# Optimization experiments

Measured on AMD Instinct MI355X. Metric: run time of the kernel, lower is better.

Reference implementation:

```python
import jax, jax.numpy as jnp
import numpy as np

MARGIN = 5.0
B, D, N_CLASSES = 384, 256, 64


def _pairwise_euclidean(emb):
    # sentence-transformers BatchHardTripletLossDistanceFunction.eucledian_distance
    dot = emb @ emb.T                          # [B,B]
    sq = jnp.diag(dot)                         # [B]
    d2 = sq[None, :] - 2.0 * dot + sq[:, None]
    d2 = jnp.maximum(d2, 0.0)
    zero = (d2 == 0.0).astype(emb.dtype)
    # add eps where zero to keep sqrt grad finite, then zero those entries
    return (1.0 - zero) * jnp.sqrt(d2 + zero * 1e-16)


def _triplet_mask(labels):
    # valid (i,j,k): distinct indices, label[i]==label[j], label[i]!=label[k]
    n = labels.shape[0]
    neq = ~jnp.eye(n, dtype=bool)
    distinct = neq[:, :, None] & neq[:, None, :] & neq[None, :, :]
    leq = labels[:, None] == labels[None, :]
    valid = leq[:, :, None] & (~leq[:, None, :])
    return valid & distinct


def setup_inputs() -> dict:
    key = jax.random.key(0)
    k1, k2 = jax.random.split(key)
    emb = jax.random.normal(k1, (B, D), dtype=jnp.float32)
    labels = jax.random.randint(k2, (B,), 0, N_CLASSES, dtype=jnp.int64)
    return {"emb": emb, "labels": labels}


def reference(emb, labels):
    pdist = _pairwise_euclidean(emb)                      # [B,B]
    # anchor-positive dist minus anchor-negative dist + margin -> [B,B,B]
    tl = pdist[:, :, None] - pdist[:, None, :] + MARGIN
    mask = _triplet_mask(labels).astype(tl.dtype)
    tl = jnp.maximum(mask * tl, 0.0)
    num_pos = jnp.sum(tl > 1e-16).astype(tl.dtype)
    return jnp.sum(tl) / (num_pos + 1e-16)
```

## Files before the change

### kernel.cpp

```cpp
#include <hip/hip_runtime.h>
#include <math.h>

#define MARGIN 5.0f
#define NB 384
#define ND 256
#define NBLK 192
#define APB 2
#define DC 32
#define NCH (ND / DC)
#define RP 33
#define MAGIC_A 0x51B7A5E1u
#define MAGIC_B 0xC3D2E1F0u

__global__ __launch_bounds__(384) void fused_kernel(const float* __restrict__ emb,
                                                    const int* __restrict__ labels,
                                                    unsigned long long* __restrict__ slotA,
                                                    unsigned long long* __restrict__ slotB,
                                                    float* __restrict__ out) {
    __shared__ float s_tile[NB][RP];
    __shared__ float s_ea[APB][ND];
    __shared__ float s_rowd[APB][NB];
    __shared__ int   s_plist[64];
    __shared__ int   s_cnt;
    __shared__ float s_red[12];

    const int i0 = blockIdx.x * APB;
    const int t  = threadIdx.x;
    const int w  = t >> 6;
    const int l  = t & 63;

    for (int x = t; x < APB * ND; x += 384)
        s_ea[x >> 8][x & (ND - 1)] = emb[(size_t)(i0 + (x >> 8)) * ND + (x & (ND - 1))];

    float acc0 = 0.f, acc1 = 0.f;
    const int rbase = (w << 6) + (l >> 3);
    const int dq    = (l & 7) << 2;

    for (int c = 0; c < NCH; ++c) {
        __syncthreads();
        #pragma unroll
        for (int q = 0; q < 8; ++q) {
            const int r = rbase + (q << 3);
            const float4 v = *(const float4*)(emb + (size_t)r * ND + c * DC + dq);
            s_tile[r][dq]     = v.x;
            s_tile[r][dq + 1] = v.y;
            s_tile[r][dq + 2] = v.z;
            s_tile[r][dq + 3] = v.w;
        }
        __syncthreads();
        #pragma unroll
        for (int d = 0; d < DC; ++d) {
            const float ev = s_tile[t][d];
            const float d0 = s_ea[0][c * DC + d] - ev;
            const float d1 = s_ea[1][c * DC + d] - ev;
            acc0 = fmaf(d0, d0, acc0);
            acc1 = fmaf(d1, d1, acc1);
        }
    }
    s_rowd[0][t] = sqrtf(acc0);
    s_rowd[1][t] = sqrtf(acc1);

    const int lt = labels[t];
    float sum = 0.f, cnt = 0.f;
    for (int a = 0; a < APB; ++a) {
        const int i  = i0 + a;
        const int li = labels[i];
        __syncthreads();
        if (t == 0) s_cnt = 0;
        __syncthreads();
        if (lt == li && t != i) {
            int p = atomicAdd(&s_cnt, 1);
            if (p < 64) s_plist[p] = t;
        }
        __syncthreads();
        const int np = (s_cnt < 64) ? s_cnt : 64;
        if (lt != li) {
            const float r1 = s_rowd[a][t];
            for (int p = 0; p < np; ++p) {
                float v = s_rowd[a][s_plist[p]] + MARGIN - r1;
                if (v > 0.f)    sum += v;
                if (v > 1e-16f) cnt += 1.f;
            }
        }
    }

    #pragma unroll
    for (int off = 32; off; off >>= 1) {
        sum += __shfl_xor(sum, off, 64);
        cnt += __shfl_xor(cnt, off, 64);
    }
    if (l == 0) { s_red[w] = sum; s_red[6 + w] = cnt; }
    __syncthreads();

    if (t == 0) {
        float ts = 0.f, tc = 0.f;
        #pragma unroll
        for (int q = 0; q < 6; ++q) { ts += s_red[q]; tc += s_red[6 + q]; }
        unsigned long long a = ((unsigned long long)MAGIC_A << 32) |
                               (unsigned long long)__float_as_uint(ts);
        unsigned long long b = ((unsigned long long)MAGIC_B << 32) |
                               (unsigned long long)__float_as_uint(tc);
        __hip_atomic_store(&slotA[blockIdx.x], a, __ATOMIC_RELEASE, __HIP_MEMORY_SCOPE_AGENT);
        __hip_atomic_store(&slotB[blockIdx.x], b, __ATOMIC_RELEASE, __HIP_MEMORY_SCOPE_AGENT);
    }

    if (blockIdx.x == 0) {
        float fs = 0.f, fc = 0.f;
        if (t < NBLK) {
            unsigned long long a, b;
            do {
                a = __hip_atomic_load(&slotA[t], __ATOMIC_ACQUIRE, __HIP_MEMORY_SCOPE_AGENT);
            } while ((unsigned)(a >> 32) != MAGIC_A);
            do {
                b = __hip_atomic_load(&slotB[t], __ATOMIC_ACQUIRE, __HIP_MEMORY_SCOPE_AGENT);
            } while ((unsigned)(b >> 32) != MAGIC_B);
            fs = __uint_as_float((unsigned)(a & 0xFFFFFFFFu));
            fc = __uint_as_float((unsigned)(b & 0xFFFFFFFFu));
            __hip_atomic_store(&slotA[t], 0ull, __ATOMIC_RELAXED, __HIP_MEMORY_SCOPE_AGENT);
            __hip_atomic_store(&slotB[t], 0ull, __ATOMIC_RELAXED, __HIP_MEMORY_SCOPE_AGENT);
        }
        __syncthreads();
        #pragma unroll
        for (int off = 32; off; off >>= 1) {
            fs += __shfl_xor(fs, off, 64);
            fc += __shfl_xor(fc, off, 64);
        }
        if (l == 0) { s_red[w] = fs; s_red[6 + w] = fc; }
        __syncthreads();
        if (t == 0) {
            float ts = 0.f, tc = 0.f;
            #pragma unroll
            for (int q = 0; q < 6; ++q) { ts += s_red[q]; tc += s_red[6 + q]; }
            out[0] = ts / (tc + 1e-16f);
        }
    }
}

extern "C" void kernel_launch(void* const* d_in, const int* in_sizes, int n_in,
                              void* d_out, int out_size, void* d_ws, size_t ws_size,
                              hipStream_t stream) {
    const float* emb    = (const float*)d_in[0];
    const int*   labels = (const int*)d_in[1];
    float*       out    = (float*)d_out;

    unsigned long long* slotA = (unsigned long long*)d_ws;
    unsigned long long* slotB = slotA + NBLK;

    fused_kernel<<<NBLK, NB, 0, stream>>>(emb, labels, slotA, slotB, out);
}
```

Before: 21.98 us.

## Double-buffer distance tiles via direct global-to-LDS loads with XOR swizzle

Replaces the register-staged LDS tile fill with global_load_lds direct copies into a double-buffered, XOR-swizzled float4 tile. The load of the next chunk overlaps compute on the current one, using manual vmcnt waits and raw barriers. Anchor rows are now read straight from global memory instead of shared. Positive-list construction for both anchors is merged into one phase, which removes per-anchor barriers, and the final spin-wait adds s_sleep. The risk is correctness of the manual waitcnt and swizzle bookkeeping, plus extra global/L1 traffic for the anchor reads.

```diff
diff --git a/kernel.cpp b/kernel.cpp
--- a/kernel.cpp
+++ b/kernel.cpp
@@ -7,77 +7,102 @@
 #define NBLK 192
 #define APB 2
 #define DC 32
-#define NCH (ND / DC)
-#define RP 33
+#define NCH 8
+#define NQ 8
 #define MAGIC_A 0x51B7A5E1u
 #define MAGIC_B 0xC3D2E1F0u
+
+__device__ __forceinline__ void gload_lds16(const float* g, void* l) {
+    __builtin_amdgcn_global_load_lds((const __attribute__((address_space(1))) void*)g,
+                                     (__attribute__((address_space(3))) void*)l, 16, 0, 0);
+}
 
 __global__ __launch_bounds__(384) void fused_kernel(const float* __restrict__ emb,
                                                     const int* __restrict__ labels,
                                                     unsigned long long* __restrict__ slotA,
                                                     unsigned long long* __restrict__ slotB,
                                                     float* __restrict__ out) {
-    __shared__ float s_tile[NB][RP];
-    __shared__ float s_ea[APB][ND];
-    __shared__ float s_rowd[APB][NB];
-    __shared__ int   s_plist[64];
-    __shared__ int   s_cnt;
-    __shared__ float s_red[12];
+    __shared__ float4 s_tile[2][NB * NQ];
+    __shared__ float  s_rowd[APB][NB];
+    __shared__ int    s_plist[APB][64];
+    __shared__ int    s_cnt[APB];
+    __shared__ float  s_red[12];
 
     const int i0 = blockIdx.x * APB;
     const int t  = threadIdx.x;
     const int w  = t >> 6;
     const int l  = t & 63;
 
-    for (int x = t; x < APB * ND; x += 384)
-        s_ea[x >> 8][x & (ND - 1)] = emb[(size_t)(i0 + (x >> 8)) * ND + (x & (ND - 1))];
+    const int lt = labels[t];
+
+    const float* gsrc0 = emb + (size_t)(w * 64 + (l >> 3)) * ND + 4 * ((l & 7) ^ (l >> 3));
+
+    const float* ea0 = emb + (size_t)(i0 + 0) * ND;
+    const float* ea1 = emb + (size_t)(i0 + 1) * ND;
 
     float acc0 = 0.f, acc1 = 0.f;
-    const int rbase = (w << 6) + (l >> 3);
-    const int dq    = (l & 7) << 2;
+    const int xk = t & 7;
+    const int tq = t * NQ;
 
+    #pragma unroll
+    for (int q = 0; q < NQ; ++q)
+        gload_lds16(gsrc0 + (size_t)q * 8 * ND, &s_tile[0][(w * NQ + q) * 64]);
+
+    #pragma unroll
     for (int c = 0; c < NCH; ++c) {
-        __syncthreads();
+        const int b = c & 1;
+        if (c + 1 < NCH) {
+            #pragma unroll
+            for (int q = 0; q < NQ; ++q)
+                gload_lds16(gsrc0 + (size_t)q * 8 * ND + (c + 1) * DC,
+                            &s_tile[b ^ 1][(w * NQ + q) * 64]);
+            asm volatile("s_waitcnt vmcnt(8)" ::: "memory");
+        } else {
+            asm volatile("s_waitcnt vmcnt(0)" ::: "memory");
+        }
+        __builtin_amdgcn_s_barrier();
+        asm volatile("" ::: "memory");
+
         #pragma unroll
-        for (int q = 0; q < 8; ++q) {
-            const int r = rbase + (q << 3);
-            const float4 v = *(const float4*)(emb + (size_t)r * ND + c * DC + dq);
-            s_tile[r][dq]     = v.x;
-            s_tile[r][dq + 1] = v.y;
-            s_tile[r][dq + 2] = v.z;
-            s_tile[r][dq + 3] = v.w;
+        for (int d4 = 0; d4 < NQ; ++d4) {
+            const float4 tv = s_tile[b][tq + (d4 ^ xk)];
+            const float4 e0 = *(const float4*)(ea0 + c * DC + 4 * d4);
+            const float4 e1 = *(const float4*)(ea1 + c * DC + 4 * d4);
+            float d;
+            d = e0.x - tv.x; acc0 = fmaf(d, d, acc0);
+            d = e0.y - tv.y; acc0 = fmaf(d, d, acc0);
+            d = e0.z - tv.z; acc0 = fmaf(d, d, acc0);
+            d = e0.w - tv.w; acc0 = fmaf(d, d, acc0);
+            d = e1.x - tv.x; acc1 = fmaf(d, d, acc1);
+            d = e1.y - tv.y; acc1 = fmaf(d, d, acc1);
+            d = e1.z - tv.z; acc1 = fmaf(d, d, acc1);
+            d = e1.w - tv.w; acc1 = fmaf(d, d, acc1);
         }
-        __syncthreads();
-        #pragma unroll
-        for (int d = 0; d < DC; ++d) {
-            const float ev = s_tile[t][d];
-            const float d0 = s_ea[0][c * DC + d] - ev;
-            const float d1 = s_ea[1][c * DC + d] - ev;
-            acc0 = fmaf(d0, d0, acc0);
-            acc1 = fmaf(d1, d1, acc1);
-        }
+        asm volatile("s_waitcnt lgkmcnt(0)" ::: "memory");
+        __builtin_amdgcn_s_barrier();
+        asm volatile("" ::: "memory");
     }
+
     s_rowd[0][t] = sqrtf(acc0);
     s_rowd[1][t] = sqrtf(acc1);
+    if (t < APB) s_cnt[t] = 0;
+    const int li0 = labels[i0];
+    const int li1 = labels[i0 + 1];
+    __syncthreads();
 
-    const int lt = labels[t];
+    if (lt == li0 && t != i0)     { int p = atomicAdd(&s_cnt[0], 1); if (p < 64) s_plist[0][p] = t; }
+    if (lt == li1 && t != i0 + 1) { int p = atomicAdd(&s_cnt[1], 1); if (p < 64) s_plist[1][p] = t; }
+    __syncthreads();
+
     float sum = 0.f, cnt = 0.f;
+    #pragma unroll
     for (int a = 0; a < APB; ++a) {
-        const int i  = i0 + a;
-        const int li = labels[i];
-        __syncthreads();
-        if (t == 0) s_cnt = 0;
-        __syncthreads();
-        if (lt == li && t != i) {
-            int p = atomicAdd(&s_cnt, 1);
-            if (p < 64) s_plist[p] = t;
-        }
-        __syncthreads();
-        const int np = (s_cnt < 64) ? s_cnt : 64;
+        const int li = a ? li1 : li0;
         if (lt != li) {
             const float r1 = s_rowd[a][t];
+            const int np = (s_cnt[a] < 64) ? s_cnt[a] : 64;
             for (int p = 0; p < np; ++p) {
-                float v = s_rowd[a][s_plist[p]] + MARGIN - r1;
+                float v = s_rowd[a][s_plist[a][p]] + MARGIN - r1;
                 if (v > 0.f)    sum += v;
                 if (v > 1e-16f) cnt += 1.f;
             }
@@ -107,13 +132,16 @@
     if (blockIdx.x == 0) {
         float fs = 0.f, fc = 0.f;
         if (t < NBLK) {
-            unsigned long long a, b;
-            do {
+            unsigned long long a = __hip_atomic_load(&slotA[t], __ATOMIC_ACQUIRE, __HIP_MEMORY_SCOPE_AGENT);
+            while ((unsigned)(a >> 32) != MAGIC_A) {
+                __builtin_amdgcn_s_sleep(2);
                 a = __hip_atomic_load(&slotA[t], __ATOMIC_ACQUIRE, __HIP_MEMORY_SCOPE_AGENT);
-            } while ((unsigned)(a >> 32) != MAGIC_A);
-            do {
+            }
+            unsigned long long b = __hip_atomic_load(&slotB[t], __ATOMIC_ACQUIRE, __HIP_MEMORY_SCOPE_AGENT);
+            while ((unsigned)(b >> 32) != MAGIC_B) {
+                __builtin_amdgcn_s_sleep(2);
                 b = __hip_atomic_load(&slotB[t], __ATOMIC_ACQUIRE, __HIP_MEMORY_SCOPE_AGENT);
-            } while ((unsigned)(b >> 32) != MAGIC_B);
+            }
             fs = __uint_as_float((unsigned)(a & 0xFFFFFFFFu));
             fc = __uint_as_float((unsigned)(b & 0xFFFFFFFFu));
             __hip_atomic_store(&slotA[t], 0ull, __ATOMIC_RELAXED, __HIP_MEMORY_SCOPE_AGENT);
```

Measured after the change: 20.30 us. 7.7% less time.
